# Optimization experiments

Measured on AMD Instinct MI355X. Metric: run time of the kernel, lower is better.

The kernel has to match this reference:

```python
import jax, jax.numpy as jnp
import numpy as np

L = 32768   # sequence length
H = 256     # dim_ssm_io
P = 128     # effective state dim = dim_ssm_state // 2 (conj_sym=True)
DT_MIN, DT_MAX = 0.001, 0.1


def setup_inputs() -> dict:
    key = jax.random.key(0)
    kB, kC, kD, kstep, ku = jax.random.split(key, 5)
    n = jnp.arange(P, dtype=jnp.float32)
    # s4d_inv initialization: Lambda = -0.5 + 1j * (P/pi) * (P/(2n+1) - 1)
    Lambda_re = -0.5 * jnp.ones((P,), dtype=jnp.float32)
    Lambda_im = (P / np.pi) * (P / (2.0 * n + 1.0) - 1.0)
    # lecun_normal over fan_in, then / sqrt(2) for conj_sym real/imag split
    B = jax.random.normal(kB, (P, H, 2), dtype=jnp.float32) / jnp.sqrt(2.0 * H)
    C = jax.random.normal(kC, (H, P, 2), dtype=jnp.float32) / jnp.sqrt(2.0 * P)
    D = jax.random.normal(kD, (H,), dtype=jnp.float32)
    log_step = (jax.random.uniform(kstep, (P,), dtype=jnp.float32)
                * (jnp.log(DT_MAX) - jnp.log(DT_MIN)) + jnp.log(DT_MIN))
    input_sequence = jax.random.normal(ku, (L, H), dtype=jnp.float32)
    return {
        "Lambda_re": Lambda_re, "Lambda_im": Lambda_im,
        "B": B, "C": C, "D": D, "log_step": log_step,
        "input_sequence": input_sequence,
    }


def reference(Lambda_re, Lambda_im, B, C, D, log_step, input_sequence):
    # assemble complex params (conj_sym path)
    Lam = Lambda_re + 1j * Lambda_im              # (P,)
    B_tilde = B[..., 0] + 1j * B[..., 1]          # (P, H)
    C_tilde = C[..., 0] + 1j * C[..., 1]          # (H, P)
    step = jnp.exp(log_step)                      # (P,)  step_rescale = 1.0
    # ZOH discretization
    Lambda_bar = jnp.exp(Lam * step)              # (P,)
    B_bar = ((Lambda_bar - 1.0) / Lam)[:, None] * B_tilde  # (P, H)
    # input projection: Bu[l] = B_bar @ u[l]
    Bu = jnp.einsum("lh,ph->lp", input_sequence.astype(B_bar.dtype), B_bar)  # (L, P)
    Lam_elems = jnp.broadcast_to(Lambda_bar, (input_sequence.shape[0], Lambda_bar.shape[0]))

    def lin_op(q_i, q_j):
        A_i, b_i = q_i
        A_j, b_j = q_j
        return (A_j * A_i, A_j * b_i + b_j)

    _, xs = jax.lax.associative_scan(lin_op, (Lam_elems, Bu))  # (L, P) complex
    # output projection with conj symmetry: 2 * Re(C_tilde @ x)
    ys = 2.0 * jnp.einsum("lp,hp->lh", xs, C_tilde).real       # (L, H)
    return ys + D * input_sequence
```

## Files before the change

kernel.cpp:

```cpp
#include <hip/hip_runtime.h>
#include <math.h>

#define L_SEQ   32768
#define H_DIM   256
#define P_DIM   128
#define P2      256
#define T_CHUNK 32
#define NBLK    1024
#define ROWS    32
#define NSEG    64
#define CPS     16

#define WS_LB    0
#define WS_A32   256
#define WS_A512  512
#define WS_COEF  768
#define WS_APOW  1024
#define WS_E     9216
#define WS_CB    271360
#define WS_PACKS 533504
#define WS_XS    664576
#define WS_S     9053184
#define WS_SC    9069568

typedef __attribute__((ext_vector_type(8))) short short8;
typedef __attribute__((ext_vector_type(4))) float f32x4;

#define SAK 264
#define STL 260

__device__ __forceinline__ void split_bf16(float v, ushort& hi, ushort& lo) {
    union { float f; unsigned u; } a; a.f = v;
    unsigned r = a.u + 0x7FFFu + ((a.u >> 16) & 1u);
    hi = (ushort)(r >> 16);
    union { unsigned u; float f; } hf; hf.u = ((unsigned)hi) << 16;
    float rem = v - hf.f;
    union { float f; unsigned u; } b; b.f = rem;
    unsigned r2 = b.u + 0x7FFFu + ((b.u >> 16) & 1u);
    lo = (ushort)(r2 >> 16);
}

__device__ __forceinline__ float4 cfma2(const float4 A, const float4 x, const float4 f) {
    float4 o;
    o.x = A.x * x.x - A.y * x.y + f.x;
    o.y = A.x * x.y + A.y * x.x + f.y;
    o.z = A.z * x.z - A.w * x.w + f.z;
    o.w = A.z * x.w + A.w * x.z + f.w;
    return o;
}

__global__ void k_setup_p(const float* __restrict__ lre, const float* __restrict__ lim,
                          const float* __restrict__ lstep, float* __restrict__ ws) {
    int p = threadIdx.x;
    if (p >= P_DIM) return;
    float step = expf(lstep[p]);
    float lr = lre[p], li = lim[p];
    double zd = (double)lr * (double)step;
    double yd = (double)li * (double)step;
    double ed = exp(zd), cd = cos(yd), sd = sin(yd);
    double lbr = ed * cd, lbi = ed * sd;
    ws[WS_LB + 2*p]     = (float)lbr;
    ws[WS_LB + 2*p + 1] = (float)lbi;
    double mr = lbr, mi = lbi;
    ws[WS_APOW + 2*p]     = (float)mr;
    ws[WS_APOW + 2*p + 1] = (float)mi;
    for (int i = 1; i < 32; i++) {
        double nr = mr * lbr - mi * lbi;
        mi = mr * lbi + mi * lbr;
        mr = nr;
        ws[WS_APOW + i*P2 + 2*p]     = (float)mr;
        ws[WS_APOW + i*P2 + 2*p + 1] = (float)mi;
    }
    ws[WS_A32 + 2*p]     = (float)mr;
    ws[WS_A32 + 2*p + 1] = (float)mi;
    double ar = mr, ai = mi;
    for (int j = 0; j < 4; j++) {
        double nr = ar*ar - ai*ai;
        ai = 2.0 * ar * ai;
        ar = nr;
    }
    ws[WS_A512 + 2*p]     = (float)ar;
    ws[WS_A512 + 2*p + 1] = (float)ai;
    float lbrf = (float)lbr, lbif = (float)lbi;
    float a = lbrf - 1.0f, b = lbif;
    float den = lr*lr + li*li;
    ws[WS_COEF + 2*p]     = (a*lr + b*li) / den;
    ws[WS_COEF + 2*p + 1] = (b*lr - a*li) / den;
}

__global__ void k_setup_mats(const float* __restrict__ B, const float* __restrict__ C,
                             const float* __restrict__ coef,
                             ushort* __restrict__ w1h, ushort* __restrict__ w1l,
                             ushort* __restrict__ w2h, ushort* __restrict__ w2l) {
    int t = blockIdx.x * blockDim.x + threadIdx.x;
    for (int e = t; e < P_DIM * H_DIM; e += 64 * 256) {
        int p = e >> 8;
        int h = e & 255;
        float br = B[(size_t)(p*H_DIM + h)*2 + 0];
        float bi = B[(size_t)(p*H_DIM + h)*2 + 1];
        float cr = coef[2*p], ci = coef[2*p + 1];
        float v1r = cr*br - ci*bi;
        float v1i = cr*bi + ci*br;
        ushort hi, lo;
        split_bf16(v1r, hi, lo);
        w1h[(size_t)(2*p)*256 + h] = hi;  w1l[(size_t)(2*p)*256 + h] = lo;
        split_bf16(v1i, hi, lo);
        w1h[(size_t)(2*p+1)*256 + h] = hi; w1l[(size_t)(2*p+1)*256 + h] = lo;
        float Cr = C[(size_t)(h*P_DIM + p)*2 + 0];
        float Ci = C[(size_t)(h*P_DIM + p)*2 + 1];
        split_bf16(2.0f*Cr, hi, lo);
        w2h[(size_t)h*256 + 2*p] = hi;    w2l[(size_t)h*256 + 2*p] = lo;
        split_bf16(-2.0f*Ci, hi, lo);
        w2h[(size_t)h*256 + 2*p+1] = hi;  w2l[(size_t)h*256 + 2*p+1] = lo;
    }
}

__global__ void k_carry_reduce(const float* __restrict__ E, float* __restrict__ S,
                               const float* __restrict__ a32) {
    const int s = blockIdx.x;
    const int q = threadIdx.x;
    const float4 A = *(const float4*)(a32 + 4 * q);
    const float* xe = E + (size_t)s * CPS * P2 + 4 * q;
    float4 e = make_float4(0.f, 0.f, 0.f, 0.f);
    #pragma unroll
    for (int j = 0; j < CPS; j++)
        e = cfma2(A, e, *(const float4*)(xe + (size_t)j * P2));
    *(float4*)(S + (size_t)s * P2 + 4 * q) = e;
}

__global__ void k_carry_scan(const float* __restrict__ S, float* __restrict__ SC,
                             const float* __restrict__ a512) {
    const int q = threadIdx.x;
    const float4 AS = *(const float4*)(a512 + 4 * q);
    float4 c = make_float4(0.f, 0.f, 0.f, 0.f);
    #pragma unroll 8
    for (int s = 0; s < NSEG; s++) {
        *(float4*)(SC + (size_t)s * P2 + 4 * q) = c;
        c = cfma2(AS, c, *(const float4*)(S + (size_t)s * P2 + 4 * q));
    }
}

__global__ void k_carry_apply(const float* __restrict__ E, const float* __restrict__ SC,
                              float* __restrict__ cb, const float* __restrict__ a32) {
    const int s = blockIdx.x;
    const int q = threadIdx.x;
    const float4 A = *(const float4*)(a32 + 4 * q);
    const float* xe = E + (size_t)s * CPS * P2 + 4 * q;
    float* cw = cb + (size_t)s * CPS * P2 + 4 * q;
    float4 c = *(const float4*)(SC + (size_t)s * P2 + 4 * q);
    #pragma unroll
    for (int j = 0; j < CPS; j++) {
        *(float4*)(cw + (size_t)j * P2) = c;
        c = cfma2(A, c, *(const float4*)(xe + (size_t)j * P2));
    }
}

template<bool EPI, bool APPLY, bool SCAN, bool BSPLIT>
__global__ __launch_bounds__(256, 4) void k_gemm_mfma(
        const float* __restrict__ A, const ushort* __restrict__ Wh,
        const ushort* __restrict__ Wl, float* __restrict__ Cmat,
        const float* __restrict__ Dv, const float* __restrict__ U,
        const float* __restrict__ ws, float* __restrict__ Eout,
        const float* __restrict__ cbin) {
    __shared__ float4 SMraw[2112];
    ushort* Ah   = (ushort*)SMraw;
    ushort* Al   = Ah + ROWS * SAK;
    float*  Tile = (float*)SMraw;

    const int t      = threadIdx.x;
    const int lane   = t & 63;
    const int wave   = t >> 6;
    const int lane16 = lane & 15;
    const int quad   = lane >> 4;
    const int blk    = blockIdx.x;
    const int l0     = blk * ROWS;

    {
        float4 f[8];
        #pragma unroll
        for (int j = 0; j < 8; j++)
            f[j] = *(const float4*)(A + (size_t)(l0 + j*4 + wave) * 256 + lane * 4);
        if (APPLY) {
            const float4 cr = *(const float4*)(cbin + (size_t)blk * P2 + lane * 4);
            #pragma unroll
            for (int j = 0; j < 8; j++) {
                const float4 ap = *(const float4*)(ws + WS_APOW + (size_t)(j*4 + wave) * P2 + lane * 4);
                f[j] = cfma2(ap, cr, f[j]);
            }
        }
        #pragma unroll
        for (int j = 0; j < 8; j++) {
            const int m = j*4 + wave;
            ushort4 h4, l4;
            split_bf16(f[j].x, h4.x, l4.x);
            split_bf16(f[j].y, h4.y, l4.y);
            split_bf16(f[j].z, h4.z, l4.z);
            split_bf16(f[j].w, h4.w, l4.w);
            *(ushort4*)(&Ah[m * SAK + lane * 4]) = h4;
            *(ushort4*)(&Al[m * SAK + lane * 4]) = l4;
        }
    }
    __syncthreads();

    f32x4 acc[2][4];
    #pragma unroll
    for (int i = 0; i < 2; i++)
        #pragma unroll
        for (int j = 0; j < 4; j++) acc[i][j] = (f32x4){0.f, 0.f, 0.f, 0.f};

    const ushort* WhB = Wh + (size_t)(wave * 64 + lane16) * 256 + quad * 8;
    const ushort* WlB = Wl + (size_t)(wave * 64 + lane16) * 256 + quad * 8;

    short8 bh[4], bl[4], nbh[4];
    #pragma unroll
    for (int nf = 0; nf < 4; nf++)
        bh[nf] = *(const short8*)(WhB + (size_t)nf * 4096);
    #pragma unroll
    for (int kt = 0; kt < 8; kt++) {
        const int k0 = kt * 32;
        if (BSPLIT) {
            #pragma unroll
            for (int nf = 0; nf < 4; nf++)
                bl[nf] = *(const short8*)(WlB + (size_t)nf * 4096 + k0);
        }
        short8 ah[2], alo[2];
        #pragma unroll
        for (int mf = 0; mf < 2; mf++) {
            int m = mf * 16 + lane16;
            ah[mf]  = *(const short8*)(&Ah[m * SAK + k0 + quad * 8]);
            alo[mf] = *(const short8*)(&Al[m * SAK + k0 + quad * 8]);
        }
        if (kt < 7) {
            #pragma unroll
            for (int nf = 0; nf < 4; nf++)
                nbh[nf] = *(const short8*)(WhB + (size_t)nf * 4096 + k0 + 32);
        }
        #pragma unroll
        for (int nf = 0; nf < 4; nf++) {
            #pragma unroll
            for (int mf = 0; mf < 2; mf++) {
                acc[mf][nf] = __builtin_amdgcn_mfma_f32_16x16x32_bf16(ah[mf],  bh[nf], acc[mf][nf], 0, 0, 0);
                if (BSPLIT)
                    acc[mf][nf] = __builtin_amdgcn_mfma_f32_16x16x32_bf16(ah[mf], bl[nf], acc[mf][nf], 0, 0, 0);
                acc[mf][nf] = __builtin_amdgcn_mfma_f32_16x16x32_bf16(alo[mf], bh[nf], acc[mf][nf], 0, 0, 0);
            }
        }
        if (kt < 7) {
            #pragma unroll
            for (int nf = 0; nf < 4; nf++) bh[nf] = nbh[nf];
        }
    }

    if (!SCAN) {
        #pragma unroll
        for (int mf = 0; mf < 2; mf++) {
            #pragma unroll
            for (int nf = 0; nf < 4; nf++) {
                int row0 = l0 + mf * 16 + quad * 4;
                int col  = wave * 64 + nf * 16 + lane16;
                #pragma unroll
                for (int r = 0; r < 4; r++) {
                    float v = acc[mf][nf][r];
                    if (EPI) v += Dv[col] * U[(size_t)(row0 + r) * 256 + col];
                    Cmat[(size_t)(row0 + r) * 256 + col] = v;
                }
            }
        }
    } else {
        __syncthreads();
        #pragma unroll
        for (int mf = 0; mf < 2; mf++)
            #pragma unroll
            for (int nf = 0; nf < 4; nf++) {
                int row = mf * 16 + quad * 4;
                int col = wave * 64 + nf * 16 + lane16;
                #pragma unroll
                for (int r = 0; r < 4; r++)
                    Tile[(row + r) * STL + col] = acc[mf][nf][r];
            }
        __syncthreads();
        if (wave == 0) {
            const float4 Alb = *(const float4*)(ws + WS_LB + 4 * lane);
            float* gbase = Cmat + (size_t)l0 * 256 + 4 * lane;
            float4 x = make_float4(0.f, 0.f, 0.f, 0.f);
            #pragma unroll 8
            for (int i = 0; i < T_CHUNK; i++) {
                const float4 f = *(const float4*)(Tile + i * STL + 4 * lane);
                x = cfma2(Alb, x, f);
                *(float4*)(gbase + (size_t)i * 256) = x;
            }
            *(float4*)(Eout + (size_t)blk * P2 + 4 * lane) = x;
        }
    }
}

extern "C" void kernel_launch(void* const* d_in, const int* in_sizes, int n_in,
                              void* d_out, int out_size, void* d_ws, size_t ws_size,
                              hipStream_t stream) {
    const float* lre   = (const float*)d_in[0];
    const float* lim   = (const float*)d_in[1];
    const float* B     = (const float*)d_in[2];
    const float* C     = (const float*)d_in[3];
    const float* D     = (const float*)d_in[4];
    const float* lstep = (const float*)d_in[5];
    const float* u     = (const float*)d_in[6];
    float* out = (float*)d_out;
    float* ws  = (float*)d_ws;
    float* xs  = ws + WS_XS;
    ushort* wpk = (ushort*)(ws + WS_PACKS);
    ushort* w1h = wpk;
    ushort* w1l = wpk + 65536;
    ushort* w2h = wpk + 131072;
    ushort* w2l = wpk + 196608;

    k_setup_p<<<1, 128, 0, stream>>>(lre, lim, lstep, ws);
    k_setup_mats<<<64, 256, 0, stream>>>(B, C, ws + WS_COEF, w1h, w1l, w2h, w2l);
    k_gemm_mfma<false, false, true, true><<<NBLK, 256, 0, stream>>>(
        u, w1h, w1l, xs, nullptr, nullptr, ws, ws + WS_E, nullptr);
    k_carry_reduce<<<NSEG, 64, 0, stream>>>(ws + WS_E, ws + WS_S, ws + WS_A32);
    k_carry_scan<<<1, 64, 0, stream>>>(ws + WS_S, ws + WS_SC, ws + WS_A512);
    k_carry_apply<<<NSEG, 64, 0, stream>>>(ws + WS_E, ws + WS_SC, ws + WS_CB,
                                           ws + WS_A32);
    k_gemm_mfma<true, true, false, false><<<NBLK, 256, 0, stream>>>(
        xs, w2h, w2l, out, D, u, ws, nullptr, ws + WS_CB);
}
```

Measured before the change: 166.6 us.

## Double GEMM block to 512 threads and parallelize intra-chunk scan across waves

The fused GEMM kernel now runs 8 waves per block, each owning 32 output columns instead of 64. The serial 32-step scan done by one wave becomes a two-level scan: each wave scans 4 rows, wave 0 scans the 8 partial carries using powers of A, and all waves apply the carry. The epilogue now goes through LDS for coalesced float4 stores, the bf16 hi split uses truncation instead of rounding, and B-fragment register prefetching is dropped. This targets the serialized scan tail and low occupancy, at the cost of extra barriers and LDS traffic, and launch_bounds(512,8) may force register spills.

```diff
diff --git a/kernel.cpp b/kernel.cpp
--- a/kernel.cpp
+++ b/kernel.cpp
@@ -8,6 +8,7 @@
 #define T_CHUNK 32
 #define NBLK    1024
 #define ROWS    32
+#define TPB     512
 #define NSEG    64
 #define CPS     16
 
@@ -34,6 +35,16 @@
     unsigned r = a.u + 0x7FFFu + ((a.u >> 16) & 1u);
     hi = (ushort)(r >> 16);
     union { unsigned u; float f; } hf; hf.u = ((unsigned)hi) << 16;
+    float rem = v - hf.f;
+    union { float f; unsigned u; } b; b.f = rem;
+    unsigned r2 = b.u + 0x7FFFu + ((b.u >> 16) & 1u);
+    lo = (ushort)(r2 >> 16);
+}
+
+__device__ __forceinline__ void split_bf16_fast(float v, ushort& hi, ushort& lo) {
+    union { float f; unsigned u; } a; a.f = v;
+    hi = (ushort)(a.u >> 16);
+    union { unsigned u; float f; } hf; hf.u = a.u & 0xFFFF0000u;
     float rem = v - hf.f;
     union { float f; unsigned u; } b; b.f = rem;
     unsigned r2 = b.u + 0x7FFFu + ((b.u >> 16) & 1u);
@@ -156,7 +167,7 @@
 }
 
 template<bool EPI, bool APPLY, bool SCAN, bool BSPLIT>
-__global__ __launch_bounds__(256, 4) void k_gemm_mfma(
+__global__ __launch_bounds__(TPB, 8) void k_gemm_mfma(
         const float* __restrict__ A, const ushort* __restrict__ Wh,
         const ushort* __restrict__ Wl, float* __restrict__ Cmat,
         const float* __restrict__ Dv, const float* __restrict__ U,
@@ -176,53 +187,44 @@
     const int l0     = blk * ROWS;
 
     {
-        float4 f[8];
-        #pragma unroll
-        for (int j = 0; j < 8; j++)
-            f[j] = *(const float4*)(A + (size_t)(l0 + j*4 + wave) * 256 + lane * 4);
+        float4 f[4];
+        #pragma unroll
+        for (int j = 0; j < 4; j++)
+            f[j] = *(const float4*)(A + (size_t)(l0 + j*8 + wave) * 256 + lane * 4);
         if (APPLY) {
             const float4 cr = *(const float4*)(cbin + (size_t)blk * P2 + lane * 4);
             #pragma unroll
-            for (int j = 0; j < 8; j++) {
-                const float4 ap = *(const float4*)(ws + WS_APOW + (size_t)(j*4 + wave) * P2 + lane * 4);
+            for (int j = 0; j < 4; j++) {
+                const float4 ap = *(const float4*)(ws + WS_APOW + (size_t)(j*8 + wave) * P2 + lane * 4);
                 f[j] = cfma2(ap, cr, f[j]);
             }
         }
         #pragma unroll
-        for (int j = 0; j < 8; j++) {
-            const int m = j*4 + wave;
+        for (int j = 0; j < 4; j++) {
+            const int m = j*8 + wave;
             ushort4 h4, l4;
-            split_bf16(f[j].x, h4.x, l4.x);
-            split_bf16(f[j].y, h4.y, l4.y);
-            split_bf16(f[j].z, h4.z, l4.z);
-            split_bf16(f[j].w, h4.w, l4.w);
+            split_bf16_fast(f[j].x, h4.x, l4.x);
+            split_bf16_fast(f[j].y, h4.y, l4.y);
+            split_bf16_fast(f[j].z, h4.z, l4.z);
+            split_bf16_fast(f[j].w, h4.w, l4.w);
             *(ushort4*)(&Ah[m * SAK + lane * 4]) = h4;
             *(ushort4*)(&Al[m * SAK + lane * 4]) = l4;
         }
     }
     __syncthreads();
 
-    f32x4 acc[2][4];
+    f32x4 acc[2][2];
     #pragma unroll
     for (int i = 0; i < 2; i++)
         #pragma unroll
-        for (int j = 0; j < 4; j++) acc[i][j] = (f32x4){0.f, 0.f, 0.f, 0.f};
-
-    const ushort* WhB = Wh + (size_t)(wave * 64 + lane16) * 256 + quad * 8;
-    const ushort* WlB = Wl + (size_t)(wave * 64 + lane16) * 256 + quad * 8;
-
-    short8 bh[4], bl[4], nbh[4];
-    #pragma unroll
-    for (int nf = 0; nf < 4; nf++)
-        bh[nf] = *(const short8*)(WhB + (size_t)nf * 4096);
+        for (int j = 0; j < 2; j++) acc[i][j] = (f32x4){0.f, 0.f, 0.f, 0.f};
+
+    const ushort* WhB = Wh + (size_t)(wave * 32 + lane16) * 256 + quad * 8;
+    const ushort* WlB = Wl + (size_t)(wave * 32 + lane16) * 256 + quad * 8;
+
     #pragma unroll
     for (int kt = 0; kt < 8; kt++) {
         const int k0 = kt * 32;
-        if (BSPLIT) {
-            #pragma unroll
-            for (int nf = 0; nf < 4; nf++)
-                bl[nf] = *(const short8*)(WlB + (size_t)nf * 4096 + k0);
-        }
         short8 ah[2], alo[2];
         #pragma unroll
         for (int mf = 0; mf < 2; mf++) {
@@ -230,67 +232,84 @@
             ah[mf]  = *(const short8*)(&Ah[m * SAK + k0 + quad * 8]);
             alo[mf] = *(const short8*)(&Al[m * SAK + k0 + quad * 8]);
         }
-        if (kt < 7) {
-            #pragma unroll
-            for (int nf = 0; nf < 4; nf++)
-                nbh[nf] = *(const short8*)(WhB + (size_t)nf * 4096 + k0 + 32);
-        }
-        #pragma unroll
-        for (int nf = 0; nf < 4; nf++) {
+        #pragma unroll
+        for (int nf = 0; nf < 2; nf++) {
+            short8 bh = *(const short8*)(WhB + (size_t)nf * 4096 + k0);
+            short8 bl;
+            if (BSPLIT) bl = *(const short8*)(WlB + (size_t)nf * 4096 + k0);
             #pragma unroll
             for (int mf = 0; mf < 2; mf++) {
-                acc[mf][nf] = __builtin_amdgcn_mfma_f32_16x16x32_bf16(ah[mf],  bh[nf], acc[mf][nf], 0, 0, 0);
+                acc[mf][nf] = __builtin_amdgcn_mfma_f32_16x16x32_bf16(ah[mf],  bh, acc[mf][nf], 0, 0, 0);
                 if (BSPLIT)
-                    acc[mf][nf] = __builtin_amdgcn_mfma_f32_16x16x32_bf16(ah[mf], bl[nf], acc[mf][nf], 0, 0, 0);
-                acc[mf][nf] = __builtin_amdgcn_mfma_f32_16x16x32_bf16(alo[mf], bh[nf], acc[mf][nf], 0, 0, 0);
+                    acc[mf][nf] = __builtin_amdgcn_mfma_f32_16x16x32_bf16(ah[mf], bl, acc[mf][nf], 0, 0, 0);
+                acc[mf][nf] = __builtin_amdgcn_mfma_f32_16x16x32_bf16(alo[mf], bh, acc[mf][nf], 0, 0, 0);
             }
         }
-        if (kt < 7) {
+    }
+
+    __syncthreads();
+    #pragma unroll
+    for (int mf = 0; mf < 2; mf++)
+        #pragma unroll
+        for (int nf = 0; nf < 2; nf++) {
+            int row = mf * 16 + quad * 4;
+            int col = wave * 32 + nf * 16 + lane16;
             #pragma unroll
-            for (int nf = 0; nf < 4; nf++) bh[nf] = nbh[nf];
-        }
-    }
+            for (int r = 0; r < 4; r++)
+                Tile[(row + r) * STL + col] = acc[mf][nf][r];
+        }
+    __syncthreads();
 
     if (!SCAN) {
-        #pragma unroll
-        for (int mf = 0; mf < 2; mf++) {
-            #pragma unroll
-            for (int nf = 0; nf < 4; nf++) {
-                int row0 = l0 + mf * 16 + quad * 4;
-                int col  = wave * 64 + nf * 16 + lane16;
-                #pragma unroll
-                for (int r = 0; r < 4; r++) {
-                    float v = acc[mf][nf][r];
-                    if (EPI) v += Dv[col] * U[(size_t)(row0 + r) * 256 + col];
-                    Cmat[(size_t)(row0 + r) * 256 + col] = v;
-                }
+        const float4 dv = *(const float4*)(Dv + 4 * lane);
+        #pragma unroll
+        for (int r = 0; r < 4; r++) {
+            const int row = wave * 4 + r;
+            const float4 tv = *(const float4*)(Tile + row * STL + 4 * lane);
+            float4 y = tv;
+            if (EPI) {
+                const float4 uv = *(const float4*)(U + (size_t)(l0 + row) * 256 + 4 * lane);
+                y.x += dv.x * uv.x;  y.y += dv.y * uv.y;
+                y.z += dv.z * uv.z;  y.w += dv.w * uv.w;
             }
+            *(float4*)(Cmat + (size_t)(l0 + row) * 256 + 4 * lane) = y;
         }
     } else {
+        const float4 Alb = *(const float4*)(ws + WS_LB + 4 * lane);
+        const float4 Ap0 = *(const float4*)(ws + WS_APOW + 0 * P2 + 4 * lane);
+        const float4 Ap1 = *(const float4*)(ws + WS_APOW + 1 * P2 + 4 * lane);
+        const float4 Ap2 = *(const float4*)(ws + WS_APOW + 2 * P2 + 4 * lane);
+        const float4 Ap3 = *(const float4*)(ws + WS_APOW + 3 * P2 + 4 * lane);
+        const float* Trow = Tile + (wave * 4) * STL + 4 * lane;
+        float4 v0 = *(const float4*)(Trow + 0 * STL);
+        float4 v1 = cfma2(Alb, v0, *(const float4*)(Trow + 1 * STL));
+        float4 v2 = cfma2(Alb, v1, *(const float4*)(Trow + 2 * STL));
+        float4 v3 = cfma2(Alb, v2, *(const float4*)(Trow + 3 * STL));
         __syncthreads();
-        #pragma unroll
-        for (int mf = 0; mf < 2; mf++)
-            #pragma unroll
-            for (int nf = 0; nf < 4; nf++) {
-                int row = mf * 16 + quad * 4;
-                int col = wave * 64 + nf * 16 + lane16;
-                #pragma unroll
-                for (int r = 0; r < 4; r++)
-                    Tile[(row + r) * STL + col] = acc[mf][nf][r];
-            }
+        *(float4*)(Tile + wave * STL + 4 * lane) = v3;
         __syncthreads();
         if (wave == 0) {
-            const float4 Alb = *(const float4*)(ws + WS_LB + 4 * lane);
-            float* gbase = Cmat + (size_t)l0 * 256 + 4 * lane;
-            float4 x = make_float4(0.f, 0.f, 0.f, 0.f);
-            #pragma unroll 8
-            for (int i = 0; i < T_CHUNK; i++) {
-                const float4 f = *(const float4*)(Tile + i * STL + 4 * lane);
-                x = cfma2(Alb, x, f);
-                *(float4*)(gbase + (size_t)i * 256) = x;
+            float4 c = make_float4(0.f, 0.f, 0.f, 0.f);
+            #pragma unroll
+            for (int j = 0; j < 8; j++) {
+                const float4 s = *(const float4*)(Tile + j * STL + 4 * lane);
+                *(float4*)(Tile + (8 + j) * STL + 4 * lane) = c;
+                c = cfma2(Ap3, c, s);
             }
-            *(float4*)(Eout + (size_t)blk * P2 + 4 * lane) = x;
-        }
+        }
+        __syncthreads();
+        const float4 c = *(const float4*)(Tile + (8 + wave) * STL + 4 * lane);
+        const float4 y0 = cfma2(Ap0, c, v0);
+        const float4 y1 = cfma2(Ap1, c, v1);
+        const float4 y2 = cfma2(Ap2, c, v2);
+        const float4 y3 = cfma2(Ap3, c, v3);
+        float* gbase = Cmat + (size_t)(l0 + wave * 4) * 256 + 4 * lane;
+        *(float4*)(gbase + 0 * 256) = y0;
+        *(float4*)(gbase + 1 * 256) = y1;
+        *(float4*)(gbase + 2 * 256) = y2;
+        *(float4*)(gbase + 3 * 256) = y3;
+        if (wave == 7)
+            *(float4*)(Eout + (size_t)blk * P2 + 4 * lane) = y3;
     }
 }
 
@@ -315,12 +334,12 @@
 
     k_setup_p<<<1, 128, 0, stream>>>(lre, lim, lstep, ws);
     k_setup_mats<<<64, 256, 0, stream>>>(B, C, ws + WS_COEF, w1h, w1l, w2h, w2l);
-    k_gemm_mfma<false, false, true, true><<<NBLK, 256, 0, stream>>>(
+    k_gemm_mfma<false, false, true, true><<<NBLK, TPB, 0, stream>>>(
         u, w1h, w1l, xs, nullptr, nullptr, ws, ws + WS_E, nullptr);
     k_carry_reduce<<<NSEG, 64, 0, stream>>>(ws + WS_E, ws + WS_S, ws + WS_A32);
     k_carry_scan<<<1, 64, 0, stream>>>(ws + WS_S, ws + WS_SC, ws + WS_A512);
     k_carry_apply<<<NSEG, 64, 0, stream>>>(ws + WS_E, ws + WS_SC, ws + WS_CB,
                                            ws + WS_A32);
-    k_gemm_mfma<true, true, false, false><<<NBLK, 256, 0, stream>>>(
+    k_gemm_mfma<true, true, false, false><<<NBLK, TPB, 0, stream>>>(
         xs, w2h, w2l, out, D, u, ws, nullptr, ws + WS_CB);
 }
```

Result: no change. 167.8 us (+0.7%).
